# Performance work log

Hardware: AMD Instinct MI355X
Metric: run time of the kernel (lower is better)

The kernel has to match this reference:

```python
import jax, jax.numpy as jnp
import numpy as np

BS, SEQ, FT_IN = 64, 576, 768
HID, HEADS, FT_OUT = 512, 4, 512
N = SEQ + 1  # pooled node + tokens
NUM_NODES = BS * N


def _build_edges():
    # star graph per sample: 0 <-> (1+j) both directions, then self loops, batched with offsets
    j = np.arange(SEQ)
    src = np.empty(2 * SEQ, np.int32); dst = np.empty(2 * SEQ, np.int32)
    src[0::2] = 0;      dst[0::2] = 1 + j
    src[1::2] = 1 + j;  dst[1::2] = 0
    loops = np.arange(N, dtype=np.int32)
    src = np.concatenate([src, loops]); dst = np.concatenate([dst, loops])
    offs = (np.arange(BS, dtype=np.int32) * N)[:, None]
    return (src[None, :] + offs).reshape(-1), (dst[None, :] + offs).reshape(-1)


def setup_inputs() -> dict:
    key = jax.random.key(0)
    ks = jax.random.split(key, 24)
    s = 0.02
    src, dst = _build_edges()
    return {
        "hidden_states": jax.random.normal(ks[0], (BS, SEQ, FT_IN), jnp.float32),
        "pooled_output": jax.random.normal(ks[1], (BS, HID), jnp.float32),
        # SeqLinear projector: 768 -> 512 -> 512
        "pw1": jax.random.normal(ks[2], (FT_IN, HID)) * s, "pb1": jnp.zeros((HID,)),
        "pw2": jax.random.normal(ks[3], (HID, HID)) * s, "pb2": jnp.zeros((HID,)),
        # GATv2 conv1: 512 -> 4 heads x 128
        "wl1": jax.random.normal(ks[4], (HID, HID)) * s, "bl1": jnp.zeros((HID,)),
        "wr1": jax.random.normal(ks[5], (HID, HID)) * s, "br1": jnp.zeros((HID,)),
        "att1": jax.random.normal(ks[6], (HEADS, HID // HEADS)) * s,
        "bias1": jnp.zeros((HID,)),
        # GATv2 conv2: 512 -> 1 head x 512
        "wl2": jax.random.normal(ks[7], (HID, HID)) * s, "bl2": jnp.zeros((HID,)),
        "wr2": jax.random.normal(ks[8], (HID, HID)) * s, "br2": jnp.zeros((HID,)),
        "att2": jax.random.normal(ks[9], (1, HID)) * s,
        "bias2": jnp.zeros((HID,)),
        # final lin: 512 -> 512
        "linw": jax.random.normal(ks[10], (HID, FT_OUT)) * s, "linb": jnp.zeros((FT_OUT,)),
        "src": jnp.asarray(src), "dst": jnp.asarray(dst),
    }


def _gatv2(x, src, dst, wl, bl, wr, br, att, bias, heads, cout, num_nodes):
    # PyG GATv2Conv (share_weights=False), eval mode (attn dropout off)
    xl = (x @ wl + bl).reshape(num_nodes, heads, cout)  # source transform (messages)
    xr = (x @ wr + br).reshape(num_nodes, heads, cout)  # target transform
    z = jax.nn.leaky_relu(xl[src] + xr[dst], negative_slope=0.2)  # [E,H,C]
    e = jnp.einsum('ehc,hc->eh', z, att)                          # [E,H]
    m = jax.ops.segment_max(e, dst, num_segments=num_nodes)
    p = jnp.exp(e - m[dst])
    s = jax.ops.segment_sum(p, dst, num_segments=num_nodes)
    alpha = p / (s[dst] + 1e-16)                                  # segment softmax over in-edges
    out = jax.ops.segment_sum(xl[src] * alpha[..., None], dst, num_segments=num_nodes)
    return out.reshape(num_nodes, heads * cout) + bias


def reference(hidden_states, pooled_output, pw1, pb1, pw2, pb2,
              wl1, bl1, wr1, br1, att1, bias1,
              wl2, bl2, wr2, br2, att2, bias2,
              linw, linb, src, dst):
    bs, seq, _ = hidden_states.shape
    n = seq + 1
    num_nodes = bs * n
    # ProjLayers / SeqLinear (eval: dropout identity); GELU between layers
    h = jax.nn.gelu(hidden_states @ pw1 + pb1)
    h = h @ pw2 + pb2                                    # [bs, seq, 512]
    x = jnp.concatenate([pooled_output[:, None, :], h], axis=1)  # [bs, n, 512]
    x = x.reshape(num_nodes, -1)
    # GNN: GATv2 -> GELU -> GATv2
    h1 = jax.nn.gelu(_gatv2(x, src, dst, wl1, bl1, wr1, br1, att1, bias1, HEADS, HID // HEADS, num_nodes))
    h2 = _gatv2(h1, src, dst, wl2, bl2, wr2, br2, att2, bias2, 1, HID, num_nodes)
    h2b = h2.reshape(bs, n, -1)
    graph_mean = h2b.mean(axis=1)                        # global_mean_pool (contiguous graphs)
    cls = h2b[:, 0, :]                                   # node 0 per graph; dropout off (eval)
    out = cls @ linw + linb + pooled_output
    return out, graph_mean
```

## Files before the change

kernel.cpp:

```cpp
#include <hip/hip_runtime.h>
#include <hip/hip_bf16.h>
#include <math.h>

constexpr int BSZ       = 64;
constexpr int SEQL      = 576;
constexpr int FTIN      = 768;
constexpr int HID       = 512;
constexpr int NNODE     = SEQL + 1;
constexpr int NUM_NODES = BSZ * NNODE;
constexpr int MROWS     = BSZ * SEQL;

using b8 = __attribute__((ext_vector_type(8))) __bf16;
using f4 = __attribute__((ext_vector_type(4))) float;

__device__ __forceinline__ float gelu_f(float x) {
    float x3 = x * x * x;
    return 0.5f * x * (1.0f + tanhf(0.7978845608028654f * (x + 0.044715f * x3)));
}
__device__ __forceinline__ float lrelu(float x) {
    return x > 0.0f ? x : 0.2f * x;
}
__device__ __forceinline__ unsigned short f2bf(float v) {
    __hip_bfloat16 b = __float2bfloat16(v);
    return __builtin_bit_cast(unsigned short, b);
}
__device__ __forceinline__ float bf2f(unsigned short u) {
    return __bfloat162float(__builtin_bit_cast(__hip_bfloat16, u));
}
__device__ __forceinline__ void split_bf(float v, unsigned short& h, unsigned short& l) {
    h = f2bf(v);
    l = f2bf(v - bf2f(h));
}
__device__ __forceinline__ void gl16(const void* g, void* l) {
    __builtin_amdgcn_global_load_lds(
        (const __attribute__((address_space(1))) unsigned int*)g,
        (__attribute__((address_space(3))) unsigned int*)l, 16, 0, 0);
}
__device__ __forceinline__ f4 mfma16(b8 a, b8 b, f4 c) {
    return __builtin_amdgcn_mfma_f32_16x16x32_bf16(a, b, c, 0, 0, 0);
}

__global__ __launch_bounds__(256) void transpose_split_k(
    const float* __restrict__ W, unsigned short* __restrict__ Th,
    unsigned short* __restrict__ Tl, int K, int N)
{
    __shared__ float t[64][65];
    const int kb = blockIdx.x * 64, nb = blockIdx.y * 64;
    for (int i = threadIdx.x; i < 64 * 64; i += 256) {
        int r = i >> 6, c = i & 63;
        t[r][c] = W[(size_t)(kb + r) * N + nb + c];
    }
    __syncthreads();
    for (int i = threadIdx.x; i < 64 * 64; i += 256) {
        int r = i >> 6, c = i & 63;
        float v = t[c][r];
        unsigned short h, l; split_bf(v, h, l);
        Th[(size_t)(nb + r) * K + kb + c] = h;
        Tl[(size_t)(nb + r) * K + kb + c] = l;
    }
}

template<int MODE, bool AF32>
__global__ __launch_bounds__(256) void bgemm(
    const unsigned short* __restrict__ Ah, const unsigned short* __restrict__ Al,
    const float* __restrict__ Af,
    const unsigned short* __restrict__ BTh, const unsigned short* __restrict__ BTl,
    const float* __restrict__ bias,
    float* __restrict__ Cf, unsigned short* __restrict__ Ch, unsigned short* __restrict__ Cl,
    int M, int K)
{
    __shared__ unsigned short ldsA_h[128 * 32], ldsA_l[128 * 32];
    __shared__ unsigned short ldsB_h[128 * 32], ldsB_l[128 * 32];

    const int tid  = threadIdx.x;
    const int wid  = tid >> 6, lane = tid & 63;
    const int wr   = wid >> 1, wc = wid & 1;
    const int lrow = lane & 15, lk = lane >> 4;
    const int row0 = blockIdx.x * 128, col0 = blockIdx.y * 128;

    f4 acc[4][4] = {};

    for (int k0 = 0; k0 < K; k0 += 32) {
        __syncthreads();

#pragma unroll
        for (int i = 0; i < 2; i++) {
            const int s = wid * 128 + i * 64 + lane;
            const int r = s >> 2, g = s & 3;
            const size_t goff = (size_t)(col0 + r) * K + k0 + g * 8;
            const int lbase = (wid * 128 + i * 64) * 8;
            gl16(BTh + goff, ldsB_h + lbase);
            gl16(BTl + goff, ldsB_l + lbase);
        }
        if constexpr (!AF32) {
#pragma unroll
            for (int i = 0; i < 2; i++) {
                const int s = wid * 128 + i * 64 + lane;
                const int r = s >> 2, g = s & 3;
                int grow = row0 + r; if (grow >= M) grow = M - 1;
                const size_t goff = (size_t)grow * K + k0 + g * 8;
                const int lbase = (wid * 128 + i * 64) * 8;
                gl16(Ah + goff, ldsA_h + lbase);
                gl16(Al + goff, ldsA_l + lbase);
            }
        } else {
#pragma unroll
            for (int q = 0; q < 4; q++) {
                const int ch = tid * 4 + q;
                const int r = ch >> 3, c4 = ch & 7;
                const float4 v = *(const float4*)(Af + (size_t)(row0 + r) * K + k0 + c4 * 4);
                unsigned short h0, l0, h1, l1, h2, l2, h3, l3;
                split_bf(v.x, h0, l0); split_bf(v.y, h1, l1);
                split_bf(v.z, h2, l2); split_bf(v.w, h3, l3);
                *(ushort4*)&ldsA_h[r * 32 + c4 * 4] = make_ushort4(h0, h1, h2, h3);
                *(ushort4*)&ldsA_l[r * 32 + c4 * 4] = make_ushort4(l0, l1, l2, l3);
            }
        }
        __syncthreads();

        const int aoff = (wr * 64 + lrow) * 32 + lk * 8;
        const int boff = (wc * 64 + lrow) * 32 + lk * 8;
        b8 a_h[4], b_h[4], tmp[4];
#pragma unroll
        for (int m = 0; m < 4; m++) a_h[m] = *(const b8*)&ldsA_h[aoff + m * 512];
#pragma unroll
        for (int n = 0; n < 4; n++) b_h[n] = *(const b8*)&ldsB_h[boff + n * 512];
#pragma unroll
        for (int m = 0; m < 4; m++)
#pragma unroll
            for (int n = 0; n < 4; n++)
                acc[m][n] = mfma16(a_h[m], b_h[n], acc[m][n]);
#pragma unroll
        for (int m = 0; m < 4; m++) tmp[m] = *(const b8*)&ldsA_l[aoff + m * 512];
#pragma unroll
        for (int m = 0; m < 4; m++)
#pragma unroll
            for (int n = 0; n < 4; n++)
                acc[m][n] = mfma16(tmp[m], b_h[n], acc[m][n]);
#pragma unroll
        for (int n = 0; n < 4; n++) tmp[n] = *(const b8*)&ldsB_l[boff + n * 512];
#pragma unroll
        for (int m = 0; m < 4; m++)
#pragma unroll
            for (int n = 0; n < 4; n++)
                acc[m][n] = mfma16(a_h[m], tmp[n], acc[m][n]);
    }

    const int gcolbase = col0 + wc * 64;
    float biasn[4];
#pragma unroll
    for (int n = 0; n < 4; n++) biasn[n] = bias[gcolbase + n * 16 + lrow];

#pragma unroll
    for (int m = 0; m < 4; m++) {
#pragma unroll
        for (int r = 0; r < 4; r++) {
            const int grow = row0 + wr * 64 + m * 16 + lk * 4 + r;
            if (grow < M) {
#pragma unroll
                for (int n = 0; n < 4; n++) {
                    float v = acc[m][n][r] + biasn[n];
                    const int gcol = gcolbase + n * 16 + lrow;
                    if constexpr (MODE == 0) {
                        Cf[(size_t)grow * HID + gcol] = v;
                    } else {
                        if constexpr (MODE == 1) v = gelu_f(v);
                        const int orow = (MODE == 2) ? (grow + grow / SEQL + 1) : grow;
                        unsigned short h, l; split_bf(v, h, l);
                        Ch[(size_t)orow * HID + gcol] = h;
                        Cl[(size_t)orow * HID + gcol] = l;
                    }
                }
            }
        }
    }
}

__global__ void build_x_pooled(const float* __restrict__ pooled,
                               unsigned short* __restrict__ xH,
                               unsigned short* __restrict__ xL)
{
    const int b = blockIdx.x;
    const int t = threadIdx.x;
    float v = pooled[b * HID + t];
    unsigned short h, l; split_bf(v, h, l);
    xH[(size_t)(b * NNODE) * HID + t] = h;
    xL[(size_t)(b * NNODE) * HID + t] = l;
}

template<int HEADS, bool GELU, bool OSPLIT>
__global__ __launch_bounds__(256) void gat_edge_k(
    const float* __restrict__ xl, const float* __restrict__ xr,
    const float* __restrict__ att, const float* __restrict__ bias,
    float* __restrict__ outF, unsigned short* __restrict__ outH,
    unsigned short* __restrict__ outL)
{
    const int b = blockIdx.x / SEQL;
    const int j = blockIdx.x % SEQL;
    const size_t row0 = (size_t)(b * NNODE) * HID;
    const size_t rowj = (size_t)(b * NNODE + 1 + j) * HID;
    const int t = threadIdx.x;
    const int c = 2 * t;

    const float2 xl0  = *(const float2*)(xl + row0 + c);
    const float2 xljv = *(const float2*)(xl + rowj + c);
    const float2 xrjv = *(const float2*)(xr + rowj + c);
    const float2 attc = *(const float2*)(att + c);

    float e0 = attc.x * lrelu(xl0.x + xrjv.x) + attc.y * lrelu(xl0.y + xrjv.y);
    float e1 = attc.x * lrelu(xljv.x + xrjv.x) + attc.y * lrelu(xljv.y + xrjv.y);

#pragma unroll
    for (int off = 32; off; off >>= 1) {
        e0 += __shfl_down(e0, off, 64);
        e1 += __shfl_down(e1, off, 64);
    }
    __shared__ float s0[4], s1[4];
    const int w = t >> 6, lane = t & 63;
    if (lane == 0) { s0[w] = e0; s1[w] = e1; }
    __syncthreads();

    float E0, E1;
    if (HEADS == 4) { E0 = s0[w]; E1 = s1[w]; }
    else            { E0 = s0[0] + s0[1] + s0[2] + s0[3];
                      E1 = s1[0] + s1[1] + s1[2] + s1[3]; }

    const float m  = fmaxf(E0, E1);
    const float p0 = expf(E0 - m);
    const float p1 = expf(E1 - m);
    const float inv = 1.0f / (p0 + p1 + 1e-16f);
    const float a0 = p0 * inv, a1 = p1 * inv;

    float ox = a0 * xl0.x + a1 * xljv.x + bias[c + 0];
    float oy = a0 * xl0.y + a1 * xljv.y + bias[c + 1];
    if (GELU) { ox = gelu_f(ox); oy = gelu_f(oy); }
    if constexpr (OSPLIT) {
        unsigned short h0, l0, h1, l1;
        split_bf(ox, h0, l0); split_bf(oy, h1, l1);
        *(ushort2*)&outH[rowj + c] = make_ushort2(h0, h1);
        *(ushort2*)&outL[rowj + c] = make_ushort2(l0, l1);
    } else {
        *(float2*)(outF + rowj + c) = make_float2(ox, oy);
    }
}

template<int HEADS, bool GELU, bool OSPLIT>
__global__ __launch_bounds__(256) void gat_node0_k(
    const float* __restrict__ xl, const float* __restrict__ xr,
    const float* __restrict__ att, const float* __restrict__ bias,
    float* __restrict__ outF, unsigned short* __restrict__ outH,
    unsigned short* __restrict__ outL)
{
    constexpr int CH = HID / HEADS;
    const int b = blockIdx.x;
    const int h = blockIdx.y;
    const int t = threadIdx.x;
    const size_t base = (size_t)(b * NNODE) * HID;

    __shared__ float xr0s[CH];
    __shared__ float es[NNODE];
    __shared__ float red[256];

    const float* atth = att + h * CH;
    for (int c = t; c < CH; c += 256) xr0s[c] = xr[base + h * CH + c];
    __syncthreads();

    for (int s = t; s < NNODE; s += 256) {
        const float* xls = xl + base + (size_t)s * HID + h * CH;
        float e = 0.0f;
        for (int c = 0; c < CH; c += 4) {
            float4 v = *(const float4*)(xls + c);
            float4 a = *(const float4*)(atth + c);
            e = fmaf(a.x, lrelu(v.x + xr0s[c + 0]), e);
            e = fmaf(a.y, lrelu(v.y + xr0s[c + 1]), e);
            e = fmaf(a.z, lrelu(v.z + xr0s[c + 2]), e);
            e = fmaf(a.w, lrelu(v.w + xr0s[c + 3]), e);
        }
        es[s] = e;
    }
    __syncthreads();

    float m = -INFINITY;
    for (int s = t; s < NNODE; s += 256) m = fmaxf(m, es[s]);
    red[t] = m; __syncthreads();
    for (int off = 128; off; off >>= 1) {
        if (t < off) red[t] = fmaxf(red[t], red[t + off]);
        __syncthreads();
    }
    m = red[0];
    __syncthreads();

    float sum = 0.0f;
    for (int s = t; s < NNODE; s += 256) {
        float p = expf(es[s] - m);
        es[s] = p;
        sum += p;
    }
    red[t] = sum; __syncthreads();
    for (int off = 128; off; off >>= 1) {
        if (t < off) red[t] += red[t + off];
        __syncthreads();
    }
    const float invS = 1.0f / (red[0] + 1e-16f);

    for (int c = t; c < CH; c += 256) {
        float acc = 0.0f;
        for (int s = 0; s < NNODE; s++)
            acc = fmaf(es[s], xl[base + (size_t)s * HID + h * CH + c], acc);
        float o = acc * invS + bias[h * CH + c];
        if (GELU) o = gelu_f(o);
        if constexpr (OSPLIT) {
            unsigned short hh, ll; split_bf(o, hh, ll);
            outH[base + h * CH + c] = hh;
            outL[base + h * CH + c] = ll;
        } else {
            outF[base + h * CH + c] = o;
        }
    }
}

__global__ __launch_bounds__(256) void mean_k(const float* __restrict__ h2,
                                              float* __restrict__ out)
{
    const int b = blockIdx.x;
    const int c = blockIdx.y * 256 + threadIdx.x;
    const float* p = h2 + (size_t)(b * NNODE) * HID + c;
    float s = 0.0f;
    for (int i = 0; i < NNODE; i++) s += p[(size_t)i * HID];
    out[(size_t)BSZ * HID + b * HID + c] = s * (1.0f / NNODE);
}

__global__ __launch_bounds__(256) void head_k(
    const float* __restrict__ h2, const float* __restrict__ linw,
    const float* __restrict__ linb, const float* __restrict__ pooled,
    float* __restrict__ out)
{
    const int b = blockIdx.x;
    const int col = blockIdx.y * 256 + threadIdx.x;
    __shared__ float cls[HID];
    for (int k = threadIdx.x; k < HID; k += 256)
        cls[k] = h2[(size_t)(b * NNODE) * HID + k];
    __syncthreads();
    float acc = 0.0f;
    for (int k = 0; k < HID; k++)
        acc = fmaf(cls[k], linw[(size_t)k * HID + col], acc);
    out[b * HID + col] = acc + linb[col] + pooled[b * HID + col];
}

extern "C" void kernel_launch(void* const* d_in, const int* in_sizes, int n_in,
                              void* d_out, int out_size, void* d_ws, size_t ws_size,
                              hipStream_t stream)
{
    const float* hs     = (const float*)d_in[0];
    const float* pooled = (const float*)d_in[1];
    const float* pw1  = (const float*)d_in[2];  const float* pb1   = (const float*)d_in[3];
    const float* pw2  = (const float*)d_in[4];  const float* pb2   = (const float*)d_in[5];
    const float* wl1  = (const float*)d_in[6];  const float* bl1   = (const float*)d_in[7];
    const float* wr1  = (const float*)d_in[8];  const float* br1   = (const float*)d_in[9];
    const float* att1 = (const float*)d_in[10]; const float* bias1 = (const float*)d_in[11];
    const float* wl2  = (const float*)d_in[12]; const float* bl2   = (const float*)d_in[13];
    const float* wr2  = (const float*)d_in[14]; const float* br2   = (const float*)d_in[15];
    const float* att2 = (const float*)d_in[16]; const float* bias2 = (const float*)d_in[17];
    const float* linw = (const float*)d_in[18]; const float* linb  = (const float*)d_in[19];
    float* out = (float*)d_out;

    char* ws = (char*)d_ws;
    const size_t RSZ = 75637760;
    char* R0 = ws;
    char* R1 = ws + RSZ;
    char* R2 = ws + 2 * RSZ;
    unsigned short* WT = (unsigned short*)(ws + 3 * RSZ);

    unsigned short* hH = (unsigned short*)R0;
    unsigned short* hL = (unsigned short*)(R0 + (size_t)MROWS * HID * 2);
    unsigned short* xH = (unsigned short*)R1;
    unsigned short* xL = (unsigned short*)(R1 + (size_t)NUM_NODES * HID * 2);
    unsigned short* h1H = xH;
    unsigned short* h1L = xL;
    float* xl_f = (float*)R2;
    float* xr_f = (float*)R0;
    float* h2   = (float*)R1;

    unsigned short* pw1T_h = (unsigned short*)R2;
    unsigned short* pw1T_l = pw1T_h + (size_t)HID * FTIN;
    unsigned short* pw2T_h = pw1T_l + (size_t)HID * FTIN;
    unsigned short* pw2T_l = pw2T_h + (size_t)HID * HID;
    const size_t WSTEP = (size_t)HID * HID;

    const dim3 blk(256);
    const dim3 g1(MROWS / 128, 4);
    const dim3 g2((NUM_NODES + 127) / 128, 4);

    transpose_split_k<<<dim3(FTIN / 64, HID / 64), blk, 0, stream>>>(pw1, pw1T_h, pw1T_l, FTIN, HID);
    transpose_split_k<<<dim3(8, 8), blk, 0, stream>>>(pw2, pw2T_h, pw2T_l, HID, HID);
    transpose_split_k<<<dim3(8, 8), blk, 0, stream>>>(wl1, WT + 0 * WSTEP, WT + 1 * WSTEP, HID, HID);
    transpose_split_k<<<dim3(8, 8), blk, 0, stream>>>(wr1, WT + 2 * WSTEP, WT + 3 * WSTEP, HID, HID);
    transpose_split_k<<<dim3(8, 8), blk, 0, stream>>>(wl2, WT + 4 * WSTEP, WT + 5 * WSTEP, HID, HID);
    transpose_split_k<<<dim3(8, 8), blk, 0, stream>>>(wr2, WT + 6 * WSTEP, WT + 7 * WSTEP, HID, HID);

    bgemm<1, true><<<g1, blk, 0, stream>>>(nullptr, nullptr, hs, pw1T_h, pw1T_l, pb1,
                                           nullptr, hH, hL, MROWS, FTIN);
    bgemm<2, false><<<g1, blk, 0, stream>>>(hH, hL, nullptr, pw2T_h, pw2T_l, pb2,
                                            nullptr, xH, xL, MROWS, HID);
    build_x_pooled<<<dim3(BSZ), dim3(512), 0, stream>>>(pooled, xH, xL);
    bgemm<0, false><<<g2, blk, 0, stream>>>(xH, xL, nullptr, WT + 0 * WSTEP, WT + 1 * WSTEP, bl1,
                                            xl_f, nullptr, nullptr, NUM_NODES, HID);
    bgemm<0, false><<<g2, blk, 0, stream>>>(xH, xL, nullptr, WT + 2 * WSTEP, WT + 3 * WSTEP, br1,
                                            xr_f, nullptr, nullptr, NUM_NODES, HID);
    gat_edge_k<4, true, true><<<dim3(MROWS), blk, 0, stream>>>(xl_f, xr_f, att1, bias1,
                                                               nullptr, h1H, h1L);
    gat_node0_k<4, true, true><<<dim3(BSZ, 4), blk, 0, stream>>>(xl_f, xr_f, att1, bias1,
                                                                 nullptr, h1H, h1L);
    bgemm<0, false><<<g2, blk, 0, stream>>>(h1H, h1L, nullptr, WT + 4 * WSTEP, WT + 5 * WSTEP, bl2,
                                            xl_f, nullptr, nullptr, NUM_NODES, HID);
    bgemm<0, false><<<g2, blk, 0, stream>>>(h1H, h1L, nullptr, WT + 6 * WSTEP, WT + 7 * WSTEP, br2,
                                            xr_f, nullptr, nullptr, NUM_NODES, HID);
    gat_edge_k<1, false, false><<<dim3(MROWS), blk, 0, stream>>>(xl_f, xr_f, att2, bias2,
                                                                 h2, nullptr, nullptr);
    gat_node0_k<1, false, false><<<dim3(BSZ, 1), blk, 0, stream>>>(xl_f, xr_f, att2, bias2,
                                                                   h2, nullptr, nullptr);
    head_k<<<dim3(BSZ, 2), blk, 0, stream>>>(h2, linw, linb, pooled, out);
    mean_k<<<dim3(BSZ, 2), blk, 0, stream>>>(h2, out);
}
```

Before: 1.084 ms.

## Fold projector second layer into GAT weights, double-buffer GEMM, fuse L/R projections

Precomputes pw2·[wl1|wr1] and the fused bias, which removes the 512x512 projector GEMM over all tokens. The GAT left and right projections now run as one N=1024 GEMM writing both outputs, and node 0 is computed separately from the pooled vector. The GEMM gains a double-buffered LDS pipeline, a fragment-friendly LDS layout and launch_bounds(256,2). Composing the weights changes rounding order, which is a small precision risk, and weight preprocessing still runs on every call.

After: 1.164 ms. 1.07x slower.

```diff
diff --git a/kernel.cpp b/kernel.cpp
--- a/kernel.cpp
+++ b/kernel.cpp
@@ -12,6 +12,7 @@
 
 using b8 = __attribute__((ext_vector_type(8))) __bf16;
 using f4 = __attribute__((ext_vector_type(4))) float;
+typedef unsigned short u16;
 
 __device__ __forceinline__ float gelu_f(float x) {
     float x3 = x * x * x;
@@ -20,14 +21,14 @@
 __device__ __forceinline__ float lrelu(float x) {
     return x > 0.0f ? x : 0.2f * x;
 }
-__device__ __forceinline__ unsigned short f2bf(float v) {
+__device__ __forceinline__ u16 f2bf(float v) {
     __hip_bfloat16 b = __float2bfloat16(v);
-    return __builtin_bit_cast(unsigned short, b);
-}
-__device__ __forceinline__ float bf2f(unsigned short u) {
+    return __builtin_bit_cast(u16, b);
+}
+__device__ __forceinline__ float bf2f(u16 u) {
     return __bfloat162float(__builtin_bit_cast(__hip_bfloat16, u));
 }
-__device__ __forceinline__ void split_bf(float v, unsigned short& h, unsigned short& l) {
+__device__ __forceinline__ void split_bf(float v, u16& h, u16& l) {
     h = f2bf(v);
     l = f2bf(v - bf2f(h));
 }
@@ -41,8 +42,8 @@
 }
 
 __global__ __launch_bounds__(256) void transpose_split_k(
-    const float* __restrict__ W, unsigned short* __restrict__ Th,
-    unsigned short* __restrict__ Tl, int K, int N)
+    const float* __restrict__ W, u16* __restrict__ Th,
+    u16* __restrict__ Tl, int K, int N)
 {
     __shared__ float t[64][65];
     const int kb = blockIdx.x * 64, nb = blockIdx.y * 64;
@@ -54,146 +55,192 @@
     for (int i = threadIdx.x; i < 64 * 64; i += 256) {
         int r = i >> 6, c = i & 63;
         float v = t[c][r];
-        unsigned short h, l; split_bf(v, h, l);
+        u16 h, l; split_bf(v, h, l);
         Th[(size_t)(nb + r) * K + kb + c] = h;
         Tl[(size_t)(nb + r) * K + kb + c] = l;
     }
 }
 
+__global__ __launch_bounds__(256) void fuse_bias_k(
+    const float* __restrict__ pb,
+    const float* __restrict__ wA, const float* __restrict__ wB,
+    const float* __restrict__ bA, const float* __restrict__ bB,
+    float* __restrict__ out)
+{
+    const int n = blockIdx.x * 256 + threadIdx.x;
+    const float* W = (n < 512) ? wA : wB;
+    const int c = n & 511;
+    float acc = 0.0f;
+    if (pb) {
+        for (int j = 0; j < 512; j++) acc = fmaf(pb[j], W[(size_t)j * 512 + c], acc);
+    }
+    out[n] = acc + ((n < 512) ? bA[c] : bB[c]);
+}
+
+__global__ __launch_bounds__(256) void node0_proj_k(
+    const float* __restrict__ pooled,
+    const float* __restrict__ wl, const float* __restrict__ wr,
+    const float* __restrict__ bl, const float* __restrict__ br,
+    float* __restrict__ XL, float* __restrict__ XR)
+{
+    const int b = blockIdx.x;
+    const int n = blockIdx.y * 256 + threadIdx.x;
+    __shared__ float p[HID];
+    for (int k = threadIdx.x; k < HID; k += 256) p[k] = pooled[b * HID + k];
+    __syncthreads();
+    const float* W = (n < 512) ? wl : wr;
+    const int c = n & 511;
+    float acc = 0.0f;
+    for (int k = 0; k < HID; k++) acc = fmaf(p[k], W[(size_t)k * 512 + c], acc);
+    acc += (n < 512) ? bl[c] : br[c];
+    const size_t row = (size_t)b * NNODE * HID;
+    if (n < 512) XL[row + c] = acc; else XR[row + c] = acc;
+}
+
 template<int MODE, bool AF32>
-__global__ __launch_bounds__(256) void bgemm(
-    const unsigned short* __restrict__ Ah, const unsigned short* __restrict__ Al,
+__global__ __launch_bounds__(256, 2) void bgemm(
+    const u16* __restrict__ Ah, const u16* __restrict__ Al,
     const float* __restrict__ Af,
-    const unsigned short* __restrict__ BTh, const unsigned short* __restrict__ BTl,
+    const u16* __restrict__ BTh, const u16* __restrict__ BTl,
     const float* __restrict__ bias,
-    float* __restrict__ Cf, unsigned short* __restrict__ Ch, unsigned short* __restrict__ Cl,
+    float* __restrict__ CfL, float* __restrict__ CfR,
+    u16* __restrict__ Ch, u16* __restrict__ Cl,
     int M, int K)
 {
-    __shared__ unsigned short ldsA_h[128 * 32], ldsA_l[128 * 32];
-    __shared__ unsigned short ldsB_h[128 * 32], ldsB_l[128 * 32];
+    __shared__ u16 lds[2][4][4096];
 
     const int tid  = threadIdx.x;
     const int wid  = tid >> 6, lane = tid & 63;
     const int wr   = wid >> 1, wc = wid & 1;
     const int lrow = lane & 15, lk = lane >> 4;
     const int row0 = blockIdx.x * 128, col0 = blockIdx.y * 128;
+    const int nt   = K >> 5;
 
     f4 acc[4][4] = {};
-
-    for (int k0 = 0; k0 < K; k0 += 32) {
-        __syncthreads();
-
+    float4 areg[4];
+
+    auto STAGE = [&](int buf, int k0) {
 #pragma unroll
         for (int i = 0; i < 2; i++) {
-            const int s = wid * 128 + i * 64 + lane;
-            const int r = s >> 2, g = s & 3;
-            const size_t goff = (size_t)(col0 + r) * K + k0 + g * 8;
-            const int lbase = (wid * 128 + i * 64) * 8;
-            gl16(BTh + goff, ldsB_h + lbase);
-            gl16(BTl + goff, ldsB_l + lbase);
-        }
-        if constexpr (!AF32) {
-#pragma unroll
-            for (int i = 0; i < 2; i++) {
-                const int s = wid * 128 + i * 64 + lane;
-                const int r = s >> 2, g = s & 3;
-                int grow = row0 + r; if (grow >= M) grow = M - 1;
-                const size_t goff = (size_t)grow * K + k0 + g * 8;
-                const int lbase = (wid * 128 + i * 64) * 8;
-                gl16(Ah + goff, ldsA_h + lbase);
-                gl16(Al + goff, ldsA_l + lbase);
+            const int r = wid * 2 + i;
+            const int bcol = col0 + r * 16 + lrow;
+            const size_t bgo = (size_t)bcol * K + k0 + lk * 8;
+            gl16(BTh + bgo, &lds[buf][2][r * 512]);
+            gl16(BTl + bgo, &lds[buf][3][r * 512]);
+            if constexpr (!AF32) {
+                int grow = row0 + r * 16 + lrow;
+                if (grow >= M) grow = M - 1;
+                const size_t ago = (size_t)grow * K + k0 + lk * 8;
+                gl16(Ah + ago, &lds[buf][0][r * 512]);
+                gl16(Al + ago, &lds[buf][1][r * 512]);
             }
-        } else {
-#pragma unroll
-            for (int q = 0; q < 4; q++) {
-                const int ch = tid * 4 + q;
-                const int r = ch >> 3, c4 = ch & 7;
-                const float4 v = *(const float4*)(Af + (size_t)(row0 + r) * K + k0 + c4 * 4);
-                unsigned short h0, l0, h1, l1, h2, l2, h3, l3;
-                split_bf(v.x, h0, l0); split_bf(v.y, h1, l1);
-                split_bf(v.z, h2, l2); split_bf(v.w, h3, l3);
-                *(ushort4*)&ldsA_h[r * 32 + c4 * 4] = make_ushort4(h0, h1, h2, h3);
-                *(ushort4*)&ldsA_l[r * 32 + c4 * 4] = make_ushort4(l0, l1, l2, l3);
-            }
-        }
-        __syncthreads();
-
-        const int aoff = (wr * 64 + lrow) * 32 + lk * 8;
-        const int boff = (wc * 64 + lrow) * 32 + lk * 8;
+        }
+    };
+    auto ALOAD = [&](int k0) {
+#pragma unroll
+        for (int q = 0; q < 4; q++) {
+            const int ch = tid * 4 + q;
+            const int r = ch >> 3, c4 = ch & 7;
+            areg[q] = *(const float4*)(Af + (size_t)(row0 + r) * K + k0 + c4 * 4);
+        }
+    };
+    auto AWRITE = [&](int buf) {
+#pragma unroll
+        for (int q = 0; q < 4; q++) {
+            const int ch = tid * 4 + q;
+            const int r = ch >> 3, c4 = ch & 7;
+            u16 h0, l0, h1, l1, h2, l2, h3, l3;
+            split_bf(areg[q].x, h0, l0); split_bf(areg[q].y, h1, l1);
+            split_bf(areg[q].z, h2, l2); split_bf(areg[q].w, h3, l3);
+            const int off = (r >> 4) * 512 + ((c4 >> 1) * 16 + (r & 15)) * 8 + (c4 & 1) * 4;
+            *(ushort4*)&lds[buf][0][off] = make_ushort4(h0, h1, h2, h3);
+            *(ushort4*)&lds[buf][1][off] = make_ushort4(l0, l1, l2, l3);
+        }
+    };
+
+    if constexpr (AF32) { ALOAD(0); AWRITE(0); }
+    STAGE(0, 0);
+    __syncthreads();
+
+    for (int t = 0; t < nt; t++) {
+        const int cur = t & 1;
+        const bool more = (t + 1 < nt);
+        if (more) {
+            if constexpr (AF32) ALOAD((t + 1) << 5);
+            STAGE(cur ^ 1, (t + 1) << 5);
+        }
         b8 a_h[4], b_h[4], tmp[4];
 #pragma unroll
-        for (int m = 0; m < 4; m++) a_h[m] = *(const b8*)&ldsA_h[aoff + m * 512];
-#pragma unroll
-        for (int n = 0; n < 4; n++) b_h[n] = *(const b8*)&ldsB_h[boff + n * 512];
+        for (int m = 0; m < 4; m++) a_h[m] = *(const b8*)&lds[cur][0][(wr * 4 + m) * 512 + lane * 8];
+#pragma unroll
+        for (int n = 0; n < 4; n++) b_h[n] = *(const b8*)&lds[cur][2][(wc * 4 + n) * 512 + lane * 8];
 #pragma unroll
         for (int m = 0; m < 4; m++)
 #pragma unroll
             for (int n = 0; n < 4; n++)
                 acc[m][n] = mfma16(a_h[m], b_h[n], acc[m][n]);
 #pragma unroll
-        for (int m = 0; m < 4; m++) tmp[m] = *(const b8*)&ldsA_l[aoff + m * 512];
+        for (int m = 0; m < 4; m++) tmp[m] = *(const b8*)&lds[cur][1][(wr * 4 + m) * 512 + lane * 8];
 #pragma unroll
         for (int m = 0; m < 4; m++)
 #pragma unroll
             for (int n = 0; n < 4; n++)
                 acc[m][n] = mfma16(tmp[m], b_h[n], acc[m][n]);
 #pragma unroll
-        for (int n = 0; n < 4; n++) tmp[n] = *(const b8*)&ldsB_l[boff + n * 512];
+        for (int n = 0; n < 4; n++) tmp[n] = *(const b8*)&lds[cur][3][(wc * 4 + n) * 512 + lane * 8];
 #pragma unroll
         for (int m = 0; m < 4; m++)
 #pragma unroll
             for (int n = 0; n < 4; n++)
                 acc[m][n] = mfma16(a_h[m], tmp[n], acc[m][n]);
+
+        if constexpr (AF32) { if (more) AWRITE(cur ^ 1); }
+        __syncthreads();
     }
 
     const int gcolbase = col0 + wc * 64;
     float biasn[4];
-#pragma unroll
-    for (int n = 0; n < 4; n++) biasn[n] = bias[gcolbase + n * 16 + lrow];
+    if constexpr (MODE != 3) {
+#pragma unroll
+        for (int n = 0; n < 4; n++) biasn[n] = bias[gcolbase + n * 16 + lrow];
+    }
 
 #pragma unroll
     for (int m = 0; m < 4; m++) {
 #pragma unroll
         for (int r = 0; r < 4; r++) {
             const int grow = row0 + wr * 64 + m * 16 + lk * 4 + r;
-            if (grow < M) {
+            if (MODE != 5 || grow < M) {
 #pragma unroll
                 for (int n = 0; n < 4; n++) {
-                    float v = acc[m][n][r] + biasn[n];
                     const int gcol = gcolbase + n * 16 + lrow;
-                    if constexpr (MODE == 0) {
-                        Cf[(size_t)grow * HID + gcol] = v;
+                    float v = acc[m][n][r];
+                    if constexpr (MODE == 1) {
+                        v = gelu_f(v + biasn[n]);
+                        u16 h, l; split_bf(v, h, l);
+                        Ch[(size_t)grow * HID + gcol] = h;
+                        Cl[(size_t)grow * HID + gcol] = l;
+                    } else if constexpr (MODE == 3) {
+                        u16 h, l; split_bf(v, h, l);
+                        Ch[(size_t)gcol * 512 + grow] = h;
+                        Cl[(size_t)gcol * 512 + grow] = l;
                     } else {
-                        if constexpr (MODE == 1) v = gelu_f(v);
-                        const int orow = (MODE == 2) ? (grow + grow / SEQL + 1) : grow;
-                        unsigned short h, l; split_bf(v, h, l);
-                        Ch[(size_t)orow * HID + gcol] = h;
-                        Cl[(size_t)orow * HID + gcol] = l;
+                        v += biasn[n];
+                        const int orow = (MODE == 4) ? (grow + grow / SEQL + 1) : grow;
+                        if (gcol < 512) CfL[(size_t)orow * HID + gcol] = v;
+                        else            CfR[(size_t)orow * HID + gcol - 512] = v;
                     }
                 }
             }
         }
     }
-}
-
-__global__ void build_x_pooled(const float* __restrict__ pooled,
-                               unsigned short* __restrict__ xH,
-                               unsigned short* __restrict__ xL)
-{
-    const int b = blockIdx.x;
-    const int t = threadIdx.x;
-    float v = pooled[b * HID + t];
-    unsigned short h, l; split_bf(v, h, l);
-    xH[(size_t)(b * NNODE) * HID + t] = h;
-    xL[(size_t)(b * NNODE) * HID + t] = l;
 }
 
 template<int HEADS, bool GELU, bool OSPLIT>
 __global__ __launch_bounds__(256) void gat_edge_k(
     const float* __restrict__ xl, const float* __restrict__ xr,
     const float* __restrict__ att, const float* __restrict__ bias,
-    float* __restrict__ outF, unsigned short* __restrict__ outH,
-    unsigned short* __restrict__ outL)
+    float* __restrict__ outF, u16* __restrict__ outH, u16* __restrict__ outL)
 {
     const int b = blockIdx.x / SEQL;
     const int j = blockIdx.x % SEQL;
@@ -235,7 +282,7 @@
     float oy = a0 * xl0.y + a1 * xljv.y + bias[c + 1];
     if (GELU) { ox = gelu_f(ox); oy = gelu_f(oy); }
     if constexpr (OSPLIT) {
-        unsigned short h0, l0, h1, l1;
+        u16 h0, l0, h1, l1;
         split_bf(ox, h0, l0); split_bf(oy, h1, l1);
         *(ushort2*)&outH[rowj + c] = make_ushort2(h0, h1);
         *(ushort2*)&outL[rowj + c] = make_ushort2(l0, l1);
@@ -248,8 +295,7 @@
 __global__ __launch_bounds__(256) void gat_node0_k(
     const float* __restrict__ xl, const float* __restrict__ xr,
     const float* __restrict__ att, const float* __restrict__ bias,
-    float* __restrict__ outF, unsigned short* __restrict__ outH,
-    unsigned short* __restrict__ outL)
+    float* __restrict__ outF, u16* __restrict__ outH, u16* __restrict__ outL)
 {
     constexpr int CH = HID / HEADS;
     const int b = blockIdx.x;
@@ -310,7 +356,7 @@
         float o = acc * invS + bias[h * CH + c];
         if (GELU) o = gelu_f(o);
         if constexpr (OSPLIT) {
-            unsigned short hh, ll; split_bf(o, hh, ll);
+            u16 hh, ll; split_bf(o, hh, ll);
             outH[base + h * CH + c] = hh;
             outL[base + h * CH + c] = ll;
         } else {
@@ -369,55 +415,52 @@
     char* R0 = ws;
     char* R1 = ws + RSZ;
     char* R2 = ws + 2 * RSZ;
-    unsigned short* WT = (unsigned short*)(ws + 3 * RSZ);
-
-    unsigned short* hH = (unsigned short*)R0;
-    unsigned short* hL = (unsigned short*)(R0 + (size_t)MROWS * HID * 2);
-    unsigned short* xH = (unsigned short*)R1;
-    unsigned short* xL = (unsigned short*)(R1 + (size_t)NUM_NODES * HID * 2);
-    unsigned short* h1H = xH;
-    unsigned short* h1L = xL;
-    float* xl_f = (float*)R2;
-    float* xr_f = (float*)R0;
-    float* h2   = (float*)R1;
-
-    unsigned short* pw1T_h = (unsigned short*)R2;
-    unsigned short* pw1T_l = pw1T_h + (size_t)HID * FTIN;
-    unsigned short* pw2T_h = pw1T_l + (size_t)HID * FTIN;
-    unsigned short* pw2T_l = pw2T_h + (size_t)HID * HID;
-    const size_t WSTEP = (size_t)HID * HID;
+    u16*  Wr = (u16*)(ws + 3 * RSZ);
+
+    u16* hH  = (u16*)R0;
+    u16* hL  = hH + (size_t)MROWS * HID;
+    u16* h1H = (u16*)R0;
+    u16* h1L = h1H + (size_t)NUM_NODES * HID;
+    float* h2 = (float*)R0;
+    float* XL = (float*)R1;
+    float* XR = (float*)R2;
+    u16* prepBT_h = (u16*)R1;
+    u16* prepBT_l = prepBT_h + 1024 * 512;
+    u16* pw1T_h   = prepBT_l + 1024 * 512;
+    u16* pw1T_l   = pw1T_h + 512 * FTIN;
+    u16* W1Th = Wr;
+    u16* W1Tl = W1Th + 1024 * 512;
+    u16* BT2h = W1Tl + 1024 * 512;
+    u16* BT2l = BT2h + 1024 * 512;
+    float* fb1 = (float*)(BT2l + 1024 * 512);
+    float* fb2 = fb1 + 1024;
 
     const dim3 blk(256);
-    const dim3 g1(MROWS / 128, 4);
-    const dim3 g2((NUM_NODES + 127) / 128, 4);
-
-    transpose_split_k<<<dim3(FTIN / 64, HID / 64), blk, 0, stream>>>(pw1, pw1T_h, pw1T_l, FTIN, HID);
-    transpose_split_k<<<dim3(8, 8), blk, 0, stream>>>(pw2, pw2T_h, pw2T_l, HID, HID);
-    transpose_split_k<<<dim3(8, 8), blk, 0, stream>>>(wl1, WT + 0 * WSTEP, WT + 1 * WSTEP, HID, HID);
-    transpose_split_k<<<dim3(8, 8), blk, 0, stream>>>(wr1, WT + 2 * WSTEP, WT + 3 * WSTEP, HID, HID);
-    transpose_split_k<<<dim3(8, 8), blk, 0, stream>>>(wl2, WT + 4 * WSTEP, WT + 5 * WSTEP, HID, HID);
-    transpose_split_k<<<dim3(8, 8), blk, 0, stream>>>(wr2, WT + 6 * WSTEP, WT + 7 * WSTEP, HID, HID);
-
-    bgemm<1, true><<<g1, blk, 0, stream>>>(nullptr, nullptr, hs, pw1T_h, pw1T_l, pb1,
-                                           nullptr, hH, hL, MROWS, FTIN);
-    bgemm<2, false><<<g1, blk, 0, stream>>>(hH, hL, nullptr, pw2T_h, pw2T_l, pb2,
-                                            nullptr, xH, xL, MROWS, HID);
-    build_x_pooled<<<dim3(BSZ), dim3(512), 0, stream>>>(pooled, xH, xL);
-    bgemm<0, false><<<g2, blk, 0, stream>>>(xH, xL, nullptr, WT + 0 * WSTEP, WT + 1 * WSTEP, bl1,
-                                            xl_f, nullptr, nullptr, NUM_NODES, HID);
-    bgemm<0, false><<<g2, blk, 0, stream>>>(xH, xL, nullptr, WT + 2 * WSTEP, WT + 3 * WSTEP, br1,
-                                            xr_f, nullptr, nullptr, NUM_NODES, HID);
-    gat_edge_k<4, true, true><<<dim3(MROWS), blk, 0, stream>>>(xl_f, xr_f, att1, bias1,
+
+    transpose_split_k<<<dim3(8, 8), blk, 0, stream>>>(wl1, prepBT_h, prepBT_l, HID, HID);
+    transpose_split_k<<<dim3(8, 8), blk, 0, stream>>>(wr1, prepBT_h + 512 * 512, prepBT_l + 512 * 512, HID, HID);
+    transpose_split_k<<<dim3(12, 8), blk, 0, stream>>>(pw1, pw1T_h, pw1T_l, FTIN, HID);
+    transpose_split_k<<<dim3(8, 8), blk, 0, stream>>>(wl2, BT2h, BT2l, HID, HID);
+    transpose_split_k<<<dim3(8, 8), blk, 0, stream>>>(wr2, BT2h + 512 * 512, BT2l + 512 * 512, HID, HID);
+    bgemm<3, true><<<dim3(4, 8), blk, 0, stream>>>(nullptr, nullptr, pw2, prepBT_h, prepBT_l,
+                                                   nullptr, nullptr, nullptr, W1Th, W1Tl, 512, HID);
+    fuse_bias_k<<<dim3(4), blk, 0, stream>>>(pb2, wl1, wr1, bl1, br1, fb1);
+    fuse_bias_k<<<dim3(4), blk, 0, stream>>>(nullptr, wl2, wr2, bl2, br2, fb2);
+
+    bgemm<1, true><<<dim3(288, 4), blk, 0, stream>>>(nullptr, nullptr, hs, pw1T_h, pw1T_l,
+                                                     pb1, nullptr, nullptr, hH, hL, MROWS, FTIN);
+    bgemm<4, false><<<dim3(288, 8), blk, 0, stream>>>(hH, hL, nullptr, W1Th, W1Tl,
+                                                      fb1, XL, XR, nullptr, nullptr, MROWS, HID);
+    node0_proj_k<<<dim3(BSZ, 4), blk, 0, stream>>>(pooled, wl1, wr1, bl1, br1, XL, XR);
+    gat_edge_k<4, true, true><<<dim3(MROWS), blk, 0, stream>>>(XL, XR, att1, bias1,
                                                                nullptr, h1H, h1L);
-    gat_node0_k<4, true, true><<<dim3(BSZ, 4), blk, 0, stream>>>(xl_f, xr_f, att1, bias1,
+    gat_node0_k<4, true, true><<<dim3(BSZ, 4), blk, 0, stream>>>(XL, XR, att1, bias1,
                                                                  nullptr, h1H, h1L);
-    bgemm<0, false><<<g2, blk, 0, stream>>>(h1H, h1L, nullptr, WT + 4 * WSTEP, WT + 5 * WSTEP, bl2,
-                                            xl_f, nullptr, nullptr, NUM_NODES, HID);
-    bgemm<0, false><<<g2, blk, 0, stream>>>(h1H, h1L, nullptr, WT + 6 * WSTEP, WT + 7 * WSTEP, br2,
-                                            xr_f, nullptr, nullptr, NUM_NODES, HID);
-    gat_edge_k<1, false, false><<<dim3(MROWS), blk, 0, stream>>>(xl_f, xr_f, att2, bias2,
+    bgemm<5, false><<<dim3(289, 8), blk, 0, stream>>>(h1H, h1L, nullptr, BT2h, BT2l,
+                                                      fb2, XL, XR, nullptr, nullptr, NUM_NODES, HID);
+    gat_edge_k<1, false, false><<<dim3(MROWS), blk, 0, stream>>>(XL, XR, att2, bias2,
                                                                  h2, nullptr, nullptr);
-    gat_node0_k<1, false, false><<<dim3(BSZ, 1), blk, 0, stream>>>(xl_f, xr_f, att2, bias2,
+    gat_node0_k<1, false, false><<<dim3(BSZ, 1), blk, 0, stream>>>(XL, XR, att2, bias2,
                                                                    h2, nullptr, nullptr);
     head_k<<<dim3(BSZ, 2), blk, 0, stream>>>(h2, linw, linb, pooled, out);
     mean_k<<<dim3(BSZ, 2), blk, 0, stream>>>(h2, out);
```
